# Kernel tuning notes

Hardware: AMD Instinct MI355X
Metric: run time of the kernel (lower is better)

## Reference

```python
import jax, jax.numpy as jnp
import numpy as np
import math

B, L, D, H, I, MAXLEN = 4, 1024, 512, 8, 2048, 1024
HD = D // H
EPS = 1e-5


def layer_norm(x, g, b):
    m = jnp.mean(x, axis=-1, keepdims=True)
    v = jnp.mean((x - m) ** 2, axis=-1, keepdims=True)
    return (x - m) * jax.lax.rsqrt(v + EPS) * g + b


def setup_inputs() -> dict:
    key = jax.random.key(0)
    ks = jax.random.split(key, 16)
    s = 0.02
    return {
        "x": jax.random.normal(ks[0], (B, L, D), jnp.float32),
        "attention_mask": jnp.ones((B, L), dtype=bool),
        "ln1_g": jnp.ones((D,), jnp.float32),
        "ln1_b": jnp.zeros((D,), jnp.float32),
        "wq": jax.random.normal(ks[1], (D, D), jnp.float32) * s,
        "bq": jnp.zeros((D,), jnp.float32),
        "wk": jax.random.normal(ks[2], (D, D), jnp.float32) * s,
        "bk": jnp.zeros((D,), jnp.float32),
        "wv": jax.random.normal(ks[3], (D, D), jnp.float32) * s,
        "bv": jnp.zeros((D,), jnp.float32),
        "qb1": jax.random.normal(ks[4], (H, HD), jnp.float32) * s,
        "qb2": jax.random.normal(ks[5], (H, HD), jnp.float32) * s,
        "rel_k": jax.random.normal(ks[6], (2 * MAXLEN + 1, HD), jnp.float32) * s,
        "rel_v": jax.random.normal(ks[7], (2 * MAXLEN + 1, HD), jnp.float32) * s,
        "wo": jax.random.normal(ks[8], (D, D), jnp.float32) * s,
        "bo": jnp.zeros((D,), jnp.float32),
        "ln2_g": jnp.ones((D,), jnp.float32),
        "ln2_b": jnp.zeros((D,), jnp.float32),
        "ffn_ln_g": jnp.ones((D,), jnp.float32),
        "ffn_ln_b": jnp.zeros((D,), jnp.float32),
        "w_in": jax.random.normal(ks[9], (D, I), jnp.float32) * s,
        "b_in": jnp.zeros((I,), jnp.float32),
        "w_out": jax.random.normal(ks[10], (I, D), jnp.float32) * s,
        "b_out": jnp.zeros((D,), jnp.float32),
    }


def reference(x, attention_mask, ln1_g, ln1_b, wq, bq, wk, bk, wv, bv, qb1, qb2,
              rel_k, rel_v, wo, bo, ln2_g, ln2_b, ffn_ln_g, ffn_ln_b,
              w_in, b_in, w_out, b_out):
    # relative position indices: distance j - i clipped to [-MAXLEN, MAXLEN]
    pos = jnp.arange(L)
    rel_idx = jnp.clip(pos[None, :] - pos[:, None], -MAXLEN, MAXLEN) + MAXLEN  # (L,L)

    # --- attention sub-layer (pre-norm) ---
    h = layer_norm(x, ln1_g, ln1_b)
    q = (h @ wq + bq).reshape(B, L, H, HD)
    k = (h @ wk + bk).reshape(B, L, H, HD)
    v = (h @ wv + bv).reshape(B, L, H, HD)

    q1 = q + qb1  # content-to-content
    q2 = q + qb2  # content-to-position

    att1 = jnp.einsum('blhd,bmhd->bhlm', q1, k)
    pek = rel_k[rel_idx]                         # (L,L,HD)
    att2 = jnp.einsum('blhd,lmd->bhlm', q2, pek)
    att = (att1 + att2) / math.sqrt(HD)
    att = jnp.where(attention_mask[:, None, None, :], att,
                    jnp.finfo(att.dtype).min)
    probs = jax.nn.softmax(att, axis=-1)

    w1o = jnp.einsum('bhlm,bmhd->blhd', probs, v)
    pev = rel_v[rel_idx]                         # (L,L,HD)
    w2o = jnp.einsum('bhlm,lmd->blhd', probs, pev)
    attn_out = (w1o + w2o).reshape(B, L, D) @ wo + bo
    x = x + attn_out

    # --- FFN sub-layer (pre-norm; FeedForward has its own internal LN) ---
    h2 = layer_norm(x, ln2_g, ln2_b)
    f = layer_norm(h2, ffn_ln_g, ffn_ln_b)
    f = jax.nn.silu(f @ w_in + b_in) @ w_out + b_out
    return x + f
```

## Files before the change

kernel.cpp:

```cpp
#include <hip/hip_runtime.h>
#include <math.h>

#define Bb 4
#define Ll 1024
#define Dd 512
#define Hh 8
#define HDd 64
#define Ii 2048
#define Mrows 4096
#define NSPLIT 4

typedef short bf16x8 __attribute__((ext_vector_type(8)));
typedef float f32x16 __attribute__((ext_vector_type(16)));

union U4 { uint4 u; bf16x8 s; };

__constant__ int RBc[16] = {0,1,2,3,8,9,10,11,16,17,18,19,24,25,26,27};

__device__ inline unsigned short f2bf(float f) {
    unsigned u = __float_as_uint(f);
    return (unsigned short)((u + 0x7FFFu + ((u >> 16) & 1u)) >> 16);
}
__device__ inline unsigned cvt_pk_bf16(float lo, float hi) {
    unsigned r;
    asm("v_cvt_pk_bf16_f32 %0, %1, %2" : "=v"(r) : "v"(lo), "v"(hi));
    return r;
}

__global__ __launch_bounds__(256) void ln_bf(const float* __restrict__ in,
                                             const float* __restrict__ g,
                                             const float* __restrict__ b,
                                             unsigned short* __restrict__ out) {
    int row = blockIdx.x;
    const float* x = in + (size_t)row * Dd;
    int t = threadIdx.x;
    float2 v = *reinterpret_cast<const float2*>(x + t * 2);

    float s = v.x + v.y;
    #pragma unroll
    for (int off = 1; off < 64; off <<= 1) s += __shfl_xor(s, off);
    __shared__ float red[4], red2[4];
    int wave = t >> 6;
    if ((t & 63) == 0) red[wave] = s;
    __syncthreads();
    float mean = (red[0] + red[1] + red[2] + red[3]) * (1.0f / 512.0f);
    float dx = v.x - mean, dy = v.y - mean;
    float s2 = dx * dx + dy * dy;
    #pragma unroll
    for (int off = 1; off < 64; off <<= 1) s2 += __shfl_xor(s2, off);
    if ((t & 63) == 0) red2[wave] = s2;
    __syncthreads();
    float var = (red2[0] + red2[1] + red2[2] + red2[3]) * (1.0f / 512.0f);
    float r = rsqrtf(var + 1e-5f);

    float2 gg = *reinterpret_cast<const float2*>(g + t * 2);
    float2 bb = *reinterpret_cast<const float2*>(b + t * 2);
    *reinterpret_cast<unsigned*>(out + (size_t)row * Dd + t * 2) =
        cvt_pk_bf16(dx * r * gg.x + bb.x, dy * r * gg.y + bb.y);
}

__global__ __launch_bounds__(256) void ln2x_bf(const float* __restrict__ in,
                                               const float* __restrict__ g1,
                                               const float* __restrict__ b1,
                                               const float* __restrict__ g2,
                                               const float* __restrict__ b2,
                                               unsigned short* __restrict__ out) {
    int row = blockIdx.x;
    const float* x = in + (size_t)row * Dd;
    int t = threadIdx.x;
    int wave = t >> 6;
    __shared__ float rA[4], rB[4], rC[4], rD[4];
    float2 v = *reinterpret_cast<const float2*>(x + t * 2);

    float s = v.x + v.y;
    #pragma unroll
    for (int off = 1; off < 64; off <<= 1) s += __shfl_xor(s, off);
    if ((t & 63) == 0) rA[wave] = s;
    __syncthreads();
    float mean = (rA[0] + rA[1] + rA[2] + rA[3]) * (1.0f / 512.0f);
    float dx = v.x - mean, dy = v.y - mean;
    float s2 = dx * dx + dy * dy;
    #pragma unroll
    for (int off = 1; off < 64; off <<= 1) s2 += __shfl_xor(s2, off);
    if ((t & 63) == 0) rB[wave] = s2;
    __syncthreads();
    float var = (rB[0] + rB[1] + rB[2] + rB[3]) * (1.0f / 512.0f);
    float r = rsqrtf(var + 1e-5f);
    float2 gg = *reinterpret_cast<const float2*>(g1 + t * 2);
    float2 bb = *reinterpret_cast<const float2*>(b1 + t * 2);
    float y0 = dx * r * gg.x + bb.x;
    float y1 = dy * r * gg.y + bb.y;

    float t1 = y0 + y1;
    #pragma unroll
    for (int off = 1; off < 64; off <<= 1) t1 += __shfl_xor(t1, off);
    if ((t & 63) == 0) rC[wave] = t1;
    __syncthreads();
    float mean2 = (rC[0] + rC[1] + rC[2] + rC[3]) * (1.0f / 512.0f);
    float e0 = y0 - mean2, e1 = y1 - mean2;
    float t2 = e0 * e0 + e1 * e1;
    #pragma unroll
    for (int off = 1; off < 64; off <<= 1) t2 += __shfl_xor(t2, off);
    if ((t & 63) == 0) rD[wave] = t2;
    __syncthreads();
    float var2 = (rD[0] + rD[1] + rD[2] + rD[3]) * (1.0f / 512.0f);
    float r2 = rsqrtf(var2 + 1e-5f);
    float2 g2v = *reinterpret_cast<const float2*>(g2 + t * 2);
    float2 b2v = *reinterpret_cast<const float2*>(b2 + t * 2);
    *reinterpret_cast<unsigned*>(out + (size_t)row * Dd + t * 2) =
        cvt_pk_bf16(e0 * r2 * g2v.x + b2v.x, e1 * r2 * g2v.y + b2v.y);
}

__global__ __launch_bounds__(256) void rel_prep2(const float* __restrict__ rk,
                                                 const float* __restrict__ rv,
                                                 unsigned short* __restrict__ rkF,
                                                 unsigned short* __restrict__ rvF) {
    __shared__ __attribute__((aligned(16))) unsigned short A_[32][72];
    __shared__ __attribute__((aligned(16))) unsigned short B_[32][72];
    const int bp = blockIdx.x;
    const int t = threadIdx.x;
    const int row = t >> 3, seg = (t & 7) * 8;
    {
        const float* ip = rk + ((size_t)(bp * 32 + row)) * 64 + seg;
        const float* iq = rv + ((size_t)(bp * 32 + row)) * 64 + seg;
        #pragma unroll
        for (int e = 0; e < 8; ++e) {
            A_[row][seg + e] = f2bf(ip[e]);
            B_[row][seg + e] = f2bf(iq[e]);
        }
    }
    __syncthreads();
    {
        const int kt = t >> 6, lane = t & 63, i = lane & 31, h = lane >> 5;
        uint4 u = *reinterpret_cast<const uint4*>(&A_[i][kt * 16 + h * 8]);
        *reinterpret_cast<uint4*>(rkF + (((size_t)bp * 4 + kt) << 9) + lane * 8) = u;
    }
    {
        const int kt = t >> 7, a = (t >> 6) & 1, lane = t & 63, i = lane & 31, h = lane >> 5;
        union { uint4 u; unsigned short s[8]; } fr;
        #pragma unroll
        for (int e = 0; e < 8; ++e) fr.s[e] = B_[kt * 16 + h * 8 + e][i + 32 * a];
        *reinterpret_cast<uint4*>(rvF + (((size_t)bp * 4 + kt * 2 + a) << 9) + lane * 8) = fr.u;
    }
}

__global__ __launch_bounds__(256) void kv_frag(const unsigned short* __restrict__ kbf,
                                               const unsigned short* __restrict__ vbf,
                                               unsigned short* __restrict__ kF,
                                               unsigned short* __restrict__ vF) {
    __shared__ __attribute__((aligned(16))) unsigned short A_[32][72];
    __shared__ __attribute__((aligned(16))) unsigned short B_[32][72];
    const int mt = blockIdx.x, bh = blockIdx.y;
    const int t = threadIdx.x;
    const int row = t >> 3, seg = (t & 7) * 8;
    size_t src = ((size_t)bh * 1024 + mt * 32 + row) * 64 + seg;
    *reinterpret_cast<uint4*>(&A_[row][seg]) = *reinterpret_cast<const uint4*>(kbf + src);
    *reinterpret_cast<uint4*>(&B_[row][seg]) = *reinterpret_cast<const uint4*>(vbf + src);
    __syncthreads();
    const size_t tb = ((size_t)bh * 32 + mt) * 2048;
    {
        const int kt = t >> 6, lane = t & 63, i = lane & 31, h = lane >> 5;
        uint4 u = *reinterpret_cast<const uint4*>(&A_[i][kt * 16 + h * 8]);
        *reinterpret_cast<uint4*>(kF + tb + kt * 512 + lane * 8) = u;
    }
    {
        const int kt = t >> 7, a = (t >> 6) & 1, lane = t & 63, i = lane & 31, h = lane >> 5;
        union { uint4 u; unsigned short s[8]; } fr;
        #pragma unroll
        for (int e = 0; e < 8; ++e) fr.s[e] = B_[kt * 16 + h * 8 + e][i + 32 * a];
        *reinterpret_cast<uint4*>(vF + tb + (kt * 2 + a) * 512 + lane * 8) = fr.u;
    }
}

__global__ __launch_bounds__(256) void transpose_pack(const float* __restrict__ in,
                                                      unsigned short* __restrict__ out,
                                                      int R, int C) {
    __shared__ unsigned short t[64][72];
    int r0 = blockIdx.y * 64, c0 = blockIdx.x * 64;
    int tid = threadIdx.x;
    int r = tid >> 2, seg = tid & 3;
    const float* ip = in + (size_t)(r0 + r) * C + c0 + seg * 16;
    #pragma unroll
    for (int q = 0; q < 4; ++q) {
        float4 v = *reinterpret_cast<const float4*>(ip + q * 4);
        t[r][seg * 16 + q * 4 + 0] = f2bf(v.x);
        t[r][seg * 16 + q * 4 + 1] = f2bf(v.y);
        t[r][seg * 16 + q * 4 + 2] = f2bf(v.z);
        t[r][seg * 16 + q * 4 + 3] = f2bf(v.w);
    }
    __syncthreads();
    int c = tid >> 2, rs = tid & 3;
    union { uint4 u[2]; unsigned short s[16]; } o;
    #pragma unroll
    for (int q = 0; q < 16; ++q) o.s[q] = t[rs * 16 + q][c];
    unsigned short* op = out + (size_t)(c0 + c) * R + r0 + rs * 16;
    *reinterpret_cast<uint4*>(op) = o.u[0];
    *reinterpret_cast<uint4*>(op + 8) = o.u[1];
}

template <int BN, int EPI>
__global__ __launch_bounds__(256) void gemm_tile(
    const unsigned short* __restrict__ A,
    const unsigned short* __restrict__ WT,
    const float* __restrict__ b0,
    const float* __restrict__ b1,
    const float* __restrict__ b2,
    const float* __restrict__ qb1,
    const float* __restrict__ qb2,
    const float* __restrict__ resid,
    float* __restrict__ outF,
    unsigned short* __restrict__ oU1,
    unsigned short* __restrict__ oU2,
    unsigned short* __restrict__ oU3,
    unsigned short* __restrict__ oU4,
    int Ndim, int Kdim) {
    constexpr int NB = (BN == 128) ? 2 : 1;
    __shared__ __attribute__((aligned(16))) unsigned short Asl[128 * 64];
    __shared__ __attribute__((aligned(16))) unsigned short Bsl[BN * 64];
    const int tid = threadIdx.x;
    const int wave = tid >> 6, lane = tid & 63;
    const int il = lane & 31, h = lane >> 5;
    const int wr = wave >> 1, wc = wave & 1;
    const int m0 = blockIdx.y * 128;
    const int n0 = blockIdx.x * BN;
    const int Ls = lane >> 3, s16 = lane & 7;
    const int sx8 = (s16 ^ Ls) * 8;

    f32x16 acc[2][NB];
    #pragma unroll
    for (int a = 0; a < 2; ++a)
        #pragma unroll
        for (int b = 0; b < NB; ++b)
            #pragma unroll
            for (int r = 0; r < 16; ++r) acc[a][b][r] = 0.0f;

    for (int k0 = 0; k0 < Kdim; k0 += 64) {
        __syncthreads();
        #pragma unroll
        for (int c = 0; c < 4; ++c) {
            const int chunk = wave * 4 + c;
            const int row = chunk * 8 + Ls;
            const unsigned short* src = A + (size_t)(m0 + row) * Kdim + k0 + sx8;
            __builtin_amdgcn_global_load_lds(
                (const __attribute__((address_space(1))) unsigned int*)src,
                (__attribute__((address_space(3))) unsigned int*)&Asl[chunk * 512],
                16, 0, 0);
        }
        #pragma unroll
        for (int c = 0; c < NB * 2; ++c) {
            const int chunk = wave * (NB * 2) + c;
            const int row = chunk * 8 + Ls;
            const unsigned short* src = WT + (size_t)(n0 + row) * Kdim + k0 + sx8;
            __builtin_amdgcn_global_load_lds(
                (const __attribute__((address_space(1))) unsigned int*)src,
                (__attribute__((address_space(3))) unsigned int*)&Bsl[chunk * 512],
                16, 0, 0);
        }
        __syncthreads();
        #pragma unroll
        for (int kt = 0; kt < 4; ++kt) {
            U4 af[2], bf[NB];
            #pragma unroll
            for (int a = 0; a < 2; ++a) {
                const int row = wr * 64 + a * 32 + il;
                af[a].u = *reinterpret_cast<const uint4*>(
                    &Asl[row * 64 + (((kt * 2 + h) ^ (row & 7)) * 8)]);
            }
            #pragma unroll
            for (int b = 0; b < NB; ++b) {
                const int col = wc * (NB * 32) + b * 32 + il;
                bf[b].u = *reinterpret_cast<const uint4*>(
                    &Bsl[col * 64 + (((kt * 2 + h) ^ (col & 7)) * 8)]);
            }
            #pragma unroll
            for (int a = 0; a < 2; ++a)
                #pragma unroll
                for (int b = 0; b < NB; ++b)
                    acc[a][b] = __builtin_amdgcn_mfma_f32_32x32x16_bf16(
                        af[a].s, bf[b].s, acc[a][b], 0, 0, 0);
        }
    }

    const int rowb = m0 + wr * 64;
    const int colb = n0 + wc * (NB * 32);
    if constexpr (EPI == 2) {
        float bz[NB];
        #pragma unroll
        for (int b = 0; b < NB; ++b) bz[b] = b0[colb + b * 32 + il];
        #pragma unroll
        for (int a = 0; a < 2; ++a)
            #pragma unroll
            for (int r = 0; r < 16; ++r) {
                int row = rowb + a * 32 + RBc[r] + 4 * h;
                #pragma unroll
                for (int b = 0; b < NB; ++b) {
                    size_t idx = (size_t)row * Ndim + colb + b * 32 + il;
                    outF[idx] = acc[a][b][r] + bz[b] + resid[idx];
                }
            }
    } else if constexpr (EPI == 1) {
        float bz[NB];
        #pragma unroll
        for (int b = 0; b < NB; ++b) bz[b] = b0[colb + b * 32 + il];
        #pragma unroll
        for (int a = 0; a < 2; ++a)
            #pragma unroll
            for (int r = 0; r < 16; ++r) {
                int row = rowb + a * 32 + RBc[r] + 4 * h;
                #pragma unroll
                for (int b = 0; b < NB; ++b) {
                    float v = acc[a][b][r] + bz[b];
                    v = v / (1.0f + __expf(-v));
                    oU1[(size_t)row * Ndim + colb + b * 32 + il] = f2bf(v);
                }
            }
    } else {
        const int which = colb >> 9;
        const int head = (colb >> 6) & 7;
        const float* bias = (which == 0) ? b0 : ((which == 1) ? b1 : b2);
        float bz[NB], a1[NB], a2[NB];
        #pragma unroll
        for (int b = 0; b < NB; ++b) {
            int nc = (colb & 511) + b * 32 + il;
            bz[b] = bias[nc];
            a1[b] = (which == 0) ? qb1[nc] : 0.0f;
            a2[b] = (which == 0) ? qb2[nc] : 0.0f;
        }
        unsigned short* okv = (which == 1) ? oU3 : oU4;
        #pragma unroll
        for (int a = 0; a < 2; ++a)
            #pragma unroll
            for (int r = 0; r < 16; ++r) {
                int row = rowb + a * 32 + RBc[r] + 4 * h;
                int bb_ = row >> 10, l = row & 1023;
                size_t base = ((size_t)(bb_ * 8 + head) * 1024 + l) * 64;
                #pragma unroll
                for (int b = 0; b < NB; ++b) {
                    float v = acc[a][b][r] + bz[b];
                    int dc = b * 32 + il;
                    if (which == 0) {
                        oU1[base + dc] = f2bf(v + a1[b]);
                        oU2[base + dc] = f2bf(v + a2[b]);
                    } else {
                        okv[base + dc] = f2bf(v);
                    }
                }
            }
    }
}

__global__ __launch_bounds__(256) void attn_mfma(
    const unsigned short* __restrict__ q1bf,
    const unsigned short* __restrict__ q2bf,
    const unsigned short* __restrict__ kF,
    const unsigned short* __restrict__ vF,
    const unsigned short* __restrict__ rkF,
    const unsigned short* __restrict__ rvF,
    unsigned short* __restrict__ Opb, float* __restrict__ Mp, float* __restrict__ Lp) {
    static constexpr int RB[16] = {0,1,2,3,8,9,10,11,16,17,18,19,24,25,26,27};
    __shared__ char smem[4 * 9728];
    const int tid = threadIdx.x;
    const int wave = tid >> 6, lane = tid & 63;
    const int i = lane & 31, h = lane >> 5;
    const bool h1 = (h != 0);
    const int bh = blockIdx.y;
    const int split = blockIdx.z;
    const int qt = blockIdx.x * 4 + wave;
    const int l0w = qt * 32;

    char* Wl = smem + wave * 9728;
    char* Ub = Wl;
    char* Pb = Wl + 4352;

    #pragma unroll
    for (int t = 0; t < 5; ++t)
        *reinterpret_cast<uint4*>(Pb + t * 1024 + lane * 16) = make_uint4(0, 0, 0, 0);

    U4 q1f[4], q2f[4];
    {
        const unsigned short* qa = q1bf + ((size_t)(bh * Ll + l0w + i)) * 64 + h * 8;
        const unsigned short* qb = q2bf + ((size_t)(bh * Ll + l0w + i)) * 64 + h * 8;
        #pragma unroll
        for (int kt = 0; kt < 4; ++kt) {
            q1f[kt].u = *reinterpret_cast<const uint4*>(qa + kt * 16);
            q2f[kt].u = *reinterpret_cast<const uint4*>(qb + kt * 16);
        }
    }

    const int ubw = 136 * i + 8 * h;
    const int urb = 134 * i + 8 * h + 64;
    const int pwb = 142 * i + 8 * h + 64;
    const int prb = 144 * i + 16 * h;

    f32x16 acc0, acc1;
    #pragma unroll
    for (int r = 0; r < 16; ++r) { acc0[r] = 0.0f; acc1[r] = 0.0f; }
    float Mi = -INFINITY, Si = 0.0f;

    for (int mt = split * 8; mt < split * 8 + 8; ++mt) {
        const int bp = mt - qt + 31;
        const size_t tb = ((size_t)bh * 32 + mt) * 2048 + lane * 8;

        f32x16 sacc;
        #pragma unroll
        for (int r = 0; r < 16; ++r) sacc[r] = 0.0f;
        #pragma unroll
        for (int kt = 0; kt < 4; ++kt) {
            U4 kf; kf.u = *reinterpret_cast<const uint4*>(kF + tb + kt * 512);
            sacc = __builtin_amdgcn_mfma_f32_32x32x16_bf16(kf.s, q1f[kt].s, sacc, 0, 0, 0);
        }
        #pragma unroll
        for (int tmt = 0; tmt < 2; ++tmt) {
            f32x16 tacc;
            #pragma unroll
            for (int r = 0; r < 16; ++r) tacc[r] = 0.0f;
            const unsigned short* rr = rkF + (((size_t)(bp + tmt)) << 11) + lane * 8;
            #pragma unroll
            for (int kt = 0; kt < 4; ++kt) {
                U4 rf; rf.u = *reinterpret_cast<const uint4*>(rr + kt * 512);
                tacc = __builtin_amdgcn_mfma_f32_32x32x16_bf16(rf.s, q2f[kt].s, tacc, 0, 0, 0);
            }
            #pragma unroll
            for (int c = 0; c < 8; ++c) {
                unsigned pkv = cvt_pk_bf16(tacc[2 * c], tacc[2 * c + 1]);
                *reinterpret_cast<unsigned*>(Ub + ubw + 2 * RB[2 * c] + 64 * tmt) = pkv;
            }
        }
        float s[16];
        #pragma unroll
        for (int r = 0; r < 16; ++r) {
            unsigned short us = *reinterpret_cast<const unsigned short*>(Ub + urb + 2 * RB[r]);
            float s2 = __uint_as_float((unsigned)us << 16);
            s[r] = (sacc[r] + s2) * 0.125f;
        }
        float tm = s[0];
        #pragma unroll
        for (int r = 1; r < 16; ++r) tm = fmaxf(tm, s[r]);
        tm = fmaxf(tm, __shfl_xor(tm, 32));
        float newM = fmaxf(Mi, tm);
        float alpha = __expf(Mi - newM);
        float p[16], ps = 0.0f;
        #pragma unroll
        for (int r = 0; r < 16; ++r) { p[r] = __expf(s[r] - newM); ps += p[r]; }
        ps += __shfl_xor(ps, 32);
        Si = Si * alpha + ps;
        Mi = newM;
        unsigned pk[8], pkP[8];
        #pragma unroll
        for (int c = 0; c < 8; ++c) pk[c] = cvt_pk_bf16(p[2 * c], p[2 * c + 1]);
        #pragma unroll
        for (int c = 0; c < 8; ++c) pkP[c] = (unsigned)__shfl_xor((int)pk[c], 32);
        #pragma unroll
        for (int r = 0; r < 16; ++r) {
            unsigned v = (r & 1) ? (pk[r >> 1] >> 16) : (pk[r >> 1] & 0xFFFFu);
            *reinterpret_cast<unsigned short*>(Pb + pwb + 2 * RB[r]) = (unsigned short)v;
        }
        #pragma unroll
        for (int r = 0; r < 16; ++r) { acc0[r] *= alpha; acc1[r] *= alpha; }
        #pragma unroll
        for (int kt = 0; kt < 2; ++kt) {
            U4 bf_;
            bf_.u.x = h1 ? pkP[4 * kt + 2] : pk[4 * kt + 0];
            bf_.u.y = h1 ? pkP[4 * kt + 3] : pk[4 * kt + 1];
            bf_.u.z = h1 ? pk [4 * kt + 2] : pkP[4 * kt + 0];
            bf_.u.w = h1 ? pk [4 * kt + 3] : pkP[4 * kt + 1];
            U4 va, vb;
            va.u = *reinterpret_cast<const uint4*>(vF + tb + (kt * 2 + 0) * 512);
            vb.u = *reinterpret_cast<const uint4*>(vF + tb + (kt * 2 + 1) * 512);
            acc0 = __builtin_amdgcn_mfma_f32_32x32x16_bf16(va.s, bf_.s, acc0, 0, 0, 0);
            acc1 = __builtin_amdgcn_mfma_f32_32x32x16_bf16(vb.s, bf_.s, acc1, 0, 0, 0);
        }
        #pragma unroll
        for (int kt = 0; kt < 4; ++kt) {
            U4 pf; pf.u = *reinterpret_cast<const uint4*>(Pb + prb + 32 * kt);
            const unsigned short* rv = rvF + (((size_t)(bp + (kt >> 1))) << 11)
                                          + ((kt & 1) * 2) * 512 + lane * 8;
            U4 ra, rb;
            ra.u = *reinterpret_cast<const uint4*>(rv);
            rb.u = *reinterpret_cast<const uint4*>(rv + 512);
            acc0 = __builtin_amdgcn_mfma_f32_32x32x16_bf16(ra.s, pf.s, acc0, 0, 0, 0);
            acc1 = __builtin_amdgcn_mfma_f32_32x32x16_bf16(rb.s, pf.s, acc1, 0, 0, 0);
        }
    }

    asm volatile("s_waitcnt lgkmcnt(0)" ::: "memory");
    __builtin_amdgcn_sched_barrier(0);
    #pragma unroll
    for (int r = 0; r < 16; ++r) {
        *reinterpret_cast<float*>(Wl + (RB[r] + 4 * h) * 132 + i * 4) = acc0[r];
        *reinterpret_cast<float*>(Wl + (RB[r] + 4 * h + 32) * 132 + i * 4) = acc1[r];
    }
    asm volatile("s_waitcnt lgkmcnt(0)" ::: "memory");
    __builtin_amdgcn_sched_barrier(0);
    const int ro = lane >> 4, dq = (lane & 15) * 4;
    const size_t baserow = (size_t)(split * 32 + bh) * 1024 + l0w;
    #pragma unroll
    for (int pss = 0; pss < 8; ++pss) {
        int row = ro + pss * 4;
        float4 vv;
        vv.x = *reinterpret_cast<float*>(Wl + (dq + 0) * 132 + row * 4);
        vv.y = *reinterpret_cast<float*>(Wl + (dq + 1) * 132 + row * 4);
        vv.z = *reinterpret_cast<float*>(Wl + (dq + 2) * 132 + row * 4);
        vv.w = *reinterpret_cast<float*>(Wl + (dq + 3) * 132 + row * 4);
        uint2 pkv = make_uint2(cvt_pk_bf16(vv.x, vv.y), cvt_pk_bf16(vv.z, vv.w));
        *reinterpret_cast<uint2*>(Opb + (baserow + row) * 64 + dq) = pkv;
    }
    if (lane < 32) {
        Mp[baserow + lane] = Mi;
        Lp[baserow + lane] = Si;
    }
}

__global__ __launch_bounds__(256) void attn_combine(const unsigned short* __restrict__ Opb,
                                                    const float* __restrict__ Mp,
                                                    const float* __restrict__ Lp,
                                                    unsigned short* __restrict__ out) {
    int g = blockIdx.x * 32 + (threadIdx.x >> 3);
    int dg = (threadIdx.x & 7) * 8;
    float ms[NSPLIT];
    float M = -INFINITY;
    #pragma unroll
    for (int s = 0; s < NSPLIT; ++s) { ms[s] = Mp[s * 32768 + g]; M = fmaxf(M, ms[s]); }
    float S = 0.0f;
    float o[8] = {0, 0, 0, 0, 0, 0, 0, 0};
    #pragma unroll
    for (int s = 0; s < NSPLIT; ++s) {
        float w = __expf(ms[s] - M);
        S += w * Lp[s * 32768 + g];
        uint4 u = *reinterpret_cast<const uint4*>(Opb + ((size_t)(s * 32768 + g)) * 64 + dg);
        const unsigned uw[4] = {u.x, u.y, u.z, u.w};
        #pragma unroll
        for (int j = 0; j < 4; ++j) {
            o[2 * j]     += w * __uint_as_float(uw[j] << 16);
            o[2 * j + 1] += w * __uint_as_float(uw[j] & 0xFFFF0000u);
        }
    }
    float inv = 1.0f / S;
    int bb = g >> 13, hh = (g >> 10) & 7, l = g & 1023;
    unsigned short* ob = out + ((size_t)((bb << 10) + l)) * 512 + hh * 64 + dg;
    uint4 pk;
    pk.x = cvt_pk_bf16(o[0] * inv, o[1] * inv);
    pk.y = cvt_pk_bf16(o[2] * inv, o[3] * inv);
    pk.z = cvt_pk_bf16(o[4] * inv, o[5] * inv);
    pk.w = cvt_pk_bf16(o[6] * inv, o[7] * inv);
    *reinterpret_cast<uint4*>(ob) = pk;
}

extern "C" void kernel_launch(void* const* d_in, const int* in_sizes, int n_in,
                              void* d_out, int out_size, void* d_ws, size_t ws_size,
                              hipStream_t stream) {
    const float* x     = (const float*)d_in[0];
    const float* ln1_g = (const float*)d_in[2];
    const float* ln1_b = (const float*)d_in[3];
    const float* wq    = (const float*)d_in[4];
    const float* bq    = (const float*)d_in[5];
    const float* wk    = (const float*)d_in[6];
    const float* bk    = (const float*)d_in[7];
    const float* wv    = (const float*)d_in[8];
    const float* bv    = (const float*)d_in[9];
    const float* qb1   = (const float*)d_in[10];
    const float* qb2   = (const float*)d_in[11];
    const float* rel_k = (const float*)d_in[12];
    const float* rel_v = (const float*)d_in[13];
    const float* wo    = (const float*)d_in[14];
    const float* bo    = (const float*)d_in[15];
    const float* ln2_g = (const float*)d_in[16];
    const float* ln2_b = (const float*)d_in[17];
    const float* ffn_g = (const float*)d_in[18];
    const float* ffn_b = (const float*)d_in[19];
    const float* w_in  = (const float*)d_in[20];
    const float* b_in  = (const float*)d_in[21];
    const float* w_out = (const float*)d_in[22];
    const float* b_out = (const float*)d_in[23];
    float* out = (float*)d_out;

    char* ws = (char*)d_ws;
    const size_t MB = 1024 * 1024;
    unsigned short* q1bf    = (unsigned short*)(ws);
    unsigned short* attn_bf = (unsigned short*)(ws);
    unsigned short* q2bf    = (unsigned short*)(ws + 4 * MB);
    unsigned short* kF      = (unsigned short*)(ws + 8 * MB);
    unsigned short* vF      = (unsigned short*)(ws + 12 * MB);
    unsigned short* kbf     = (unsigned short*)(ws + 16 * MB);
    unsigned short* vbf     = (unsigned short*)(ws + 20 * MB);
    float*          x2      = (float*)(ws + 16 * MB);
    unsigned short* h_bf    = (unsigned short*)(ws + 24 * MB);
    unsigned short* f_bf    = (unsigned short*)(ws + 24 * MB);
    unsigned short* Opb     = (unsigned short*)(ws + 28 * MB);
    unsigned short* f1_bf   = (unsigned short*)(ws + 28 * MB);
    float*          Mp      = (float*)(ws + 44 * MB);
    float*          Lp      = (float*)(ws + 44 * MB + 512 * 1024);
    unsigned short* rkF     = (unsigned short*)(ws + 45 * MB);
    unsigned short* rvF     = (unsigned short*)(ws + 45 * MB + 262144);
    unsigned short* wqkvT   = (unsigned short*)(ws + 46 * MB);
    unsigned short* woT     = (unsigned short*)(ws + 47 * MB + 512 * 1024);
    unsigned short* winT    = (unsigned short*)(ws + 48 * MB);
    unsigned short* woutT   = (unsigned short*)(ws + 50 * MB);

    dim3 blk(256);
    dim3 gT512(8, 8);
    dim3 ga(8, 32, NSPLIT);

    transpose_pack<<<gT512, blk, 0, stream>>>(wq, wqkvT, 512, 512);
    transpose_pack<<<gT512, blk, 0, stream>>>(wk, wqkvT + 262144, 512, 512);
    transpose_pack<<<gT512, blk, 0, stream>>>(wv, wqkvT + 524288, 512, 512);
    transpose_pack<<<gT512, blk, 0, stream>>>(wo, woT, 512, 512);
    transpose_pack<<<dim3(32, 8), blk, 0, stream>>>(w_in, winT, 512, 2048);
    transpose_pack<<<dim3(8, 32), blk, 0, stream>>>(w_out, woutT, 2048, 512);
    rel_prep2<<<64, blk, 0, stream>>>(rel_k, rel_v, rkF, rvF);

    ln_bf<<<Mrows, blk, 0, stream>>>(x, ln1_g, ln1_b, h_bf);
    gemm_tile<128, 6><<<dim3(12, 32), blk, 0, stream>>>(
        h_bf, wqkvT, bq, bk, bv, qb1, qb2, nullptr,
        nullptr, q1bf, q2bf, kbf, vbf, 1536, 512);
    kv_frag<<<dim3(32, 32), blk, 0, stream>>>(kbf, vbf, kF, vF);
    attn_mfma<<<ga, blk, 0, stream>>>(q1bf, q2bf, kF, vF, rkF, rvF, Opb, Mp, Lp);
    attn_combine<<<1024, blk, 0, stream>>>(Opb, Mp, Lp, attn_bf);
    gemm_tile<64, 2><<<dim3(8, 32), blk, 0, stream>>>(
        attn_bf, woT, bo, nullptr, nullptr, nullptr, nullptr, x,
        x2, nullptr, nullptr, nullptr, nullptr, 512, 512);
    ln2x_bf<<<Mrows, blk, 0, stream>>>(x2, ln2_g, ln2_b, ffn_g, ffn_b, f_bf);
    gemm_tile<128, 1><<<dim3(16, 32), blk, 0, stream>>>(
        f_bf, winT, b_in, nullptr, nullptr, nullptr, nullptr, nullptr,
        nullptr, f1_bf, nullptr, nullptr, nullptr, 2048, 512);
    gemm_tile<64, 2><<<dim3(8, 32), blk, 0, stream>>>(
        f1_bf, woutT, b_out, nullptr, nullptr, nullptr, nullptr, x2,
        out, nullptr, nullptr, nullptr, nullptr, 512, 2048);
}
```

Baseline: 291.0 us.

## Double attention key splits, add lazy softmax rescale, write fragment-order partials

Splits the key dimension of attention across 8 blocks instead of 4 to raise occupancy. Online softmax now skips the rescale of the accumulators unless the running max grows by more than a threshold. Partial outputs are written straight from MFMA registers in fragment order, dropping the LDS transpose, and the combine kernel reads that layout instead. Four weight transposes merge into one launch, and the workspace is remapped so the FFN weight transposes can run later. The cost is more partials for the combine step to merge and a looser softmax bound that may lose accuracy if scores grow large.

```diff
diff --git a/kernel.cpp b/kernel.cpp
--- a/kernel.cpp
+++ b/kernel.cpp
@@ -8,7 +8,7 @@
 #define HDd 64
 #define Ii 2048
 #define Mrows 4096
-#define NSPLIT 4
+#define NSPLIT 8
 
 typedef short bf16x8 __attribute__((ext_vector_type(8)));
 typedef float f32x16 __attribute__((ext_vector_type(16)));
@@ -194,6 +194,42 @@
     #pragma unroll
     for (int q = 0; q < 16; ++q) o.s[q] = t[rs * 16 + q][c];
     unsigned short* op = out + (size_t)(c0 + c) * R + r0 + rs * 16;
+    *reinterpret_cast<uint4*>(op) = o.u[0];
+    *reinterpret_cast<uint4*>(op + 8) = o.u[1];
+}
+
+__global__ __launch_bounds__(256) void transpose_pack4(
+    const float* __restrict__ s0, const float* __restrict__ s1,
+    const float* __restrict__ s2, const float* __restrict__ s3,
+    unsigned short* __restrict__ d0, unsigned short* __restrict__ d1,
+    unsigned short* __restrict__ d2, unsigned short* __restrict__ d3) {
+    __shared__ unsigned short t[64][72];
+    const float* in;
+    unsigned short* out;
+    switch (blockIdx.z) {
+        case 0: in = s0; out = d0; break;
+        case 1: in = s1; out = d1; break;
+        case 2: in = s2; out = d2; break;
+        default: in = s3; out = d3; break;
+    }
+    int r0 = blockIdx.y * 64, c0 = blockIdx.x * 64;
+    int tid = threadIdx.x;
+    int r = tid >> 2, seg = tid & 3;
+    const float* ip = in + (size_t)(r0 + r) * 512 + c0 + seg * 16;
+    #pragma unroll
+    for (int q = 0; q < 4; ++q) {
+        float4 v = *reinterpret_cast<const float4*>(ip + q * 4);
+        t[r][seg * 16 + q * 4 + 0] = f2bf(v.x);
+        t[r][seg * 16 + q * 4 + 1] = f2bf(v.y);
+        t[r][seg * 16 + q * 4 + 2] = f2bf(v.z);
+        t[r][seg * 16 + q * 4 + 3] = f2bf(v.w);
+    }
+    __syncthreads();
+    int c = tid >> 2, rs = tid & 3;
+    union { uint4 u[2]; unsigned short s[16]; } o;
+    #pragma unroll
+    for (int q = 0; q < 16; ++q) o.s[q] = t[rs * 16 + q][c];
+    unsigned short* op = out + (size_t)(c0 + c) * 512 + r0 + rs * 16;
     *reinterpret_cast<uint4*>(op) = o.u[0];
     *reinterpret_cast<uint4*>(op + 8) = o.u[1];
 }
@@ -356,9 +392,9 @@
     const unsigned short* __restrict__ vF,
     const unsigned short* __restrict__ rkF,
     const unsigned short* __restrict__ rvF,
-    unsigned short* __restrict__ Opb, float* __restrict__ Mp, float* __restrict__ Lp) {
+    unsigned* __restrict__ Opb, float* __restrict__ Mp, float* __restrict__ Lp) {
     static constexpr int RB[16] = {0,1,2,3,8,9,10,11,16,17,18,19,24,25,26,27};
-    __shared__ char smem[4 * 9728];
+    __shared__ char smem[4 * 9472];
     const int tid = threadIdx.x;
     const int wave = tid >> 6, lane = tid & 63;
     const int i = lane & 31, h = lane >> 5;
@@ -368,7 +404,7 @@
     const int qt = blockIdx.x * 4 + wave;
     const int l0w = qt * 32;
 
-    char* Wl = smem + wave * 9728;
+    char* Wl = smem + wave * 9472;
     char* Ub = Wl;
     char* Pb = Wl + 4352;
 
@@ -397,7 +433,7 @@
     for (int r = 0; r < 16; ++r) { acc0[r] = 0.0f; acc1[r] = 0.0f; }
     float Mi = -INFINITY, Si = 0.0f;
 
-    for (int mt = split * 8; mt < split * 8 + 8; ++mt) {
+    for (int mt = split * 4; mt < split * 4 + 4; ++mt) {
         const int bp = mt - qt + 31;
         const size_t tb = ((size_t)bh * 32 + mt) * 2048 + lane * 8;
 
@@ -437,14 +473,19 @@
         #pragma unroll
         for (int r = 1; r < 16; ++r) tm = fmaxf(tm, s[r]);
         tm = fmaxf(tm, __shfl_xor(tm, 32));
-        float newM = fmaxf(Mi, tm);
-        float alpha = __expf(Mi - newM);
+        if (!__all(tm <= Mi + 8.0f)) {
+            float newM = fmaxf(Mi, tm);
+            float alpha = __expf(Mi - newM);
+            Si *= alpha;
+            #pragma unroll
+            for (int r = 0; r < 16; ++r) { acc0[r] *= alpha; acc1[r] *= alpha; }
+            Mi = newM;
+        }
         float p[16], ps = 0.0f;
         #pragma unroll
-        for (int r = 0; r < 16; ++r) { p[r] = __expf(s[r] - newM); ps += p[r]; }
+        for (int r = 0; r < 16; ++r) { p[r] = __expf(s[r] - Mi); ps += p[r]; }
         ps += __shfl_xor(ps, 32);
-        Si = Si * alpha + ps;
-        Mi = newM;
+        Si += ps;
         unsigned pk[8], pkP[8];
         #pragma unroll
         for (int c = 0; c < 8; ++c) pk[c] = cvt_pk_bf16(p[2 * c], p[2 * c + 1]);
@@ -455,8 +496,6 @@
             unsigned v = (r & 1) ? (pk[r >> 1] >> 16) : (pk[r >> 1] & 0xFFFFu);
             *reinterpret_cast<unsigned short*>(Pb + pwb + 2 * RB[r]) = (unsigned short)v;
         }
-        #pragma unroll
-        for (int r = 0; r < 16; ++r) { acc0[r] *= alpha; acc1[r] *= alpha; }
         #pragma unroll
         for (int kt = 0; kt < 2; ++kt) {
             U4 bf_;
@@ -483,40 +522,29 @@
         }
     }
 
-    asm volatile("s_waitcnt lgkmcnt(0)" ::: "memory");
-    __builtin_amdgcn_sched_barrier(0);
-    #pragma unroll
-    for (int r = 0; r < 16; ++r) {
-        *reinterpret_cast<float*>(Wl + (RB[r] + 4 * h) * 132 + i * 4) = acc0[r];
-        *reinterpret_cast<float*>(Wl + (RB[r] + 4 * h + 32) * 132 + i * 4) = acc1[r];
-    }
-    asm volatile("s_waitcnt lgkmcnt(0)" ::: "memory");
-    __builtin_amdgcn_sched_barrier(0);
-    const int ro = lane >> 4, dq = (lane & 15) * 4;
-    const size_t baserow = (size_t)(split * 32 + bh) * 1024 + l0w;
-    #pragma unroll
-    for (int pss = 0; pss < 8; ++pss) {
-        int row = ro + pss * 4;
-        float4 vv;
-        vv.x = *reinterpret_cast<float*>(Wl + (dq + 0) * 132 + row * 4);
-        vv.y = *reinterpret_cast<float*>(Wl + (dq + 1) * 132 + row * 4);
-        vv.z = *reinterpret_cast<float*>(Wl + (dq + 2) * 132 + row * 4);
-        vv.w = *reinterpret_cast<float*>(Wl + (dq + 3) * 132 + row * 4);
-        uint2 pkv = make_uint2(cvt_pk_bf16(vv.x, vv.y), cvt_pk_bf16(vv.z, vv.w));
-        *reinterpret_cast<uint2*>(Opb + (baserow + row) * 64 + dq) = pkv;
+    const size_t ob = (((size_t)split * 32 + bh) * 32 + qt) * 1024;
+    #pragma unroll
+    for (int c = 0; c < 8; ++c) {
+        Opb[ob + c * 64 + lane]         = cvt_pk_bf16(acc0[2 * c], acc0[2 * c + 1]);
+        Opb[ob + (8 + c) * 64 + lane]   = cvt_pk_bf16(acc1[2 * c], acc1[2 * c + 1]);
     }
     if (lane < 32) {
+        const size_t baserow = (size_t)(split * 32 + bh) * 1024 + l0w;
         Mp[baserow + lane] = Mi;
         Lp[baserow + lane] = Si;
     }
 }
 
-__global__ __launch_bounds__(256) void attn_combine(const unsigned short* __restrict__ Opb,
+__global__ __launch_bounds__(256) void attn_combine(const unsigned* __restrict__ Opb,
                                                     const float* __restrict__ Mp,
                                                     const float* __restrict__ Lp,
                                                     unsigned short* __restrict__ out) {
-    int g = blockIdx.x * 32 + (threadIdx.x >> 3);
-    int dg = (threadIdx.x & 7) * 8;
+    const int t = threadIdx.x;
+    const int g = blockIdx.x * 32 + (t >> 3);
+    const int dg = (t & 7) * 8;
+    const int i = g & 31, qt = (g >> 5) & 31, bh = g >> 10;
+    const int accsel = dg >> 5;
+    const int c0 = ((dg & 31) >> 3) * 2;
     float ms[NSPLIT];
     float M = -INFINITY;
     #pragma unroll
@@ -527,13 +555,17 @@
     for (int s = 0; s < NSPLIT; ++s) {
         float w = __expf(ms[s] - M);
         S += w * Lp[s * 32768 + g];
-        uint4 u = *reinterpret_cast<const uint4*>(Opb + ((size_t)(s * 32768 + g)) * 64 + dg);
-        const unsigned uw[4] = {u.x, u.y, u.z, u.w};
-        #pragma unroll
-        for (int j = 0; j < 4; ++j) {
-            o[2 * j]     += w * __uint_as_float(uw[j] << 16);
-            o[2 * j + 1] += w * __uint_as_float(uw[j] & 0xFFFF0000u);
-        }
+        const unsigned* bp = Opb + (((size_t)s * 32 + bh) * 32 + qt) * 1024
+                                 + accsel * 512 + c0 * 64 + i;
+        unsigned u00 = bp[0], u01 = bp[64], u10 = bp[32], u11 = bp[96];
+        o[0] += w * __uint_as_float(u00 << 16);
+        o[1] += w * __uint_as_float(u00 & 0xFFFF0000u);
+        o[2] += w * __uint_as_float(u01 << 16);
+        o[3] += w * __uint_as_float(u01 & 0xFFFF0000u);
+        o[4] += w * __uint_as_float(u10 << 16);
+        o[5] += w * __uint_as_float(u10 & 0xFFFF0000u);
+        o[6] += w * __uint_as_float(u11 << 16);
+        o[7] += w * __uint_as_float(u11 & 0xFFFF0000u);
     }
     float inv = 1.0f / S;
     int bb = g >> 13, hh = (g >> 10) & 7, l = g & 1023;
@@ -582,31 +614,27 @@
     unsigned short* kF      = (unsigned short*)(ws + 8 * MB);
     unsigned short* vF      = (unsigned short*)(ws + 12 * MB);
     unsigned short* kbf     = (unsigned short*)(ws + 16 * MB);
+    unsigned short* f_bf    = (unsigned short*)(ws + 16 * MB);
     unsigned short* vbf     = (unsigned short*)(ws + 20 * MB);
-    float*          x2      = (float*)(ws + 16 * MB);
+    float*          x2      = (float*)(ws + 20 * MB);
     unsigned short* h_bf    = (unsigned short*)(ws + 24 * MB);
-    unsigned short* f_bf    = (unsigned short*)(ws + 24 * MB);
-    unsigned short* Opb     = (unsigned short*)(ws + 28 * MB);
+    unsigned*       Opb     = (unsigned*)(ws + 28 * MB);
     unsigned short* f1_bf   = (unsigned short*)(ws + 28 * MB);
-    float*          Mp      = (float*)(ws + 44 * MB);
-    float*          Lp      = (float*)(ws + 44 * MB + 512 * 1024);
-    unsigned short* rkF     = (unsigned short*)(ws + 45 * MB);
-    unsigned short* rvF     = (unsigned short*)(ws + 45 * MB + 262144);
-    unsigned short* wqkvT   = (unsigned short*)(ws + 46 * MB);
-    unsigned short* woT     = (unsigned short*)(ws + 47 * MB + 512 * 1024);
-    unsigned short* winT    = (unsigned short*)(ws + 48 * MB);
-    unsigned short* woutT   = (unsigned short*)(ws + 50 * MB);
+    unsigned short* wqkvT   = (unsigned short*)(ws + 44 * MB);
+    unsigned short* winT    = (unsigned short*)(ws + 44 * MB);
+    unsigned short* woutT   = (unsigned short*)(ws + 46 * MB);
+    float*          Mp      = (float*)(ws + 60 * MB);
+    float*          Lp      = (float*)(ws + 61 * MB);
+    unsigned short* rkF     = (unsigned short*)(ws + 62 * MB);
+    unsigned short* rvF     = (unsigned short*)(ws + 62 * MB + 262144);
+    unsigned short* woT     = (unsigned short*)(ws + 62 * MB + 524288);
 
     dim3 blk(256);
-    dim3 gT512(8, 8);
     dim3 ga(8, 32, NSPLIT);
 
-    transpose_pack<<<gT512, blk, 0, stream>>>(wq, wqkvT, 512, 512);
-    transpose_pack<<<gT512, blk, 0, stream>>>(wk, wqkvT + 262144, 512, 512);
-    transpose_pack<<<gT512, blk, 0, stream>>>(wv, wqkvT + 524288, 512, 512);
-    transpose_pack<<<gT512, blk, 0, stream>>>(wo, woT, 512, 512);
-    transpose_pack<<<dim3(32, 8), blk, 0, stream>>>(w_in, winT, 512, 2048);
-    transpose_pack<<<dim3(8, 32), blk, 0, stream>>>(w_out, woutT, 2048, 512);
+    transpose_pack4<<<dim3(8, 8, 4), blk, 0, stream>>>(wq, wk, wv, wo,
+                                                       wqkvT, wqkvT + 262144,
+                                                       wqkvT + 524288, woT);
     rel_prep2<<<64, blk, 0, stream>>>(rel_k, rel_v, rkF, rvF);
 
     ln_bf<<<Mrows, blk, 0, stream>>>(x, ln1_g, ln1_b, h_bf);
@@ -616,6 +644,8 @@
     kv_frag<<<dim3(32, 32), blk, 0, stream>>>(kbf, vbf, kF, vF);
     attn_mfma<<<ga, blk, 0, stream>>>(q1bf, q2bf, kF, vF, rkF, rvF, Opb, Mp, Lp);
     attn_combine<<<1024, blk, 0, stream>>>(Opb, Mp, Lp, attn_bf);
+    transpose_pack<<<dim3(32, 8), blk, 0, stream>>>(w_in, winT, 512, 2048);
+    transpose_pack<<<dim3(8, 32), blk, 0, stream>>>(w_out, woutT, 2048, 512);
     gemm_tile<64, 2><<<dim3(8, 32), blk, 0, stream>>>(
         attn_bf, woT, bo, nullptr, nullptr, nullptr, nullptr, x,
         x2, nullptr, nullptr, nullptr, nullptr, 512, 512);
```

Result: no change. 285.9 us (-1.7%).
